# Optimization experiments

Hardware: AMD Instinct MI355X
Metric: run time of the kernel (lower is better)

The kernel has to match this reference:

```python
import jax, jax.numpy as jnp
import numpy as np

N0, N1 = 30000, 20000
N = N0 + N1
E = 400000
H0, H1, H2 = 4, 4, 1
DH = 64            # num_hidden
NC = 16            # num_classes
IN = 128           # per-type input feature dim
SLOPE = 0.2        # leaky relu negative slope


def setup_inputs() -> dict:
    key = jax.random.key(0)
    ks = iter(jax.random.split(key, 48))
    rn = lambda shape, s=0.05: jax.random.normal(next(ks), shape, jnp.float32) * s
    ri = lambda shape: jax.random.randint(next(ks), shape, 0, N, jnp.int32)
    inp = {
        'features0': rn((N0, IN), 1.0),
        'features1': rn((N1, IN), 1.0),
        'fc_w0': rn((IN, DH)), 'fc_b0': jnp.zeros((DH,), jnp.float32),
        'fc_w1': rn((IN, DH)), 'fc_b1': jnp.zeros((DH,), jnp.float32),
        'mix_w': jnp.zeros((2, 3, 2), jnp.float32),  # (n_types, num_layers+1, n_graphs)
        # GATConv params stacked over the 2 relation graphs
        'W0': rn((2, DH, H0 * DH)), 'al0': rn((2, H0, DH), 0.1), 'ar0': rn((2, H0, DH), 0.1), 'b0': jnp.zeros((2, H0 * DH), jnp.float32),
        'W1': rn((2, H0 * DH, H1 * DH)), 'al1': rn((2, H1, DH), 0.1), 'ar1': rn((2, H1, DH), 0.1), 'b1': jnp.zeros((2, H1 * DH), jnp.float32),
        'W2': rn((2, H1 * DH, H2 * NC)), 'al2': rn((2, H2, NC), 0.1), 'ar2': rn((2, H2, NC), 0.1), 'b2': jnp.zeros((2, H2 * NC), jnp.float32),
        'res2': rn((2, H1 * DH, H2 * NC)),  # res_fc for last layer (in != out*heads)
        'src0': ri((E,)), 'dst0': ri((E,)),
        'src1': ri((E,)), 'dst1': ri((E,)),
    }
    return inp


def gat_conv(h, src, dst, W, al, ar, b, H, D, res_mode, res_w, act):
    # h: (N, in)  ->  (N, H, D)
    feat = (h @ W).reshape(N, H, D)
    el = jnp.sum(feat * al, axis=-1)   # (N, H)
    er = jnp.sum(feat * ar, axis=-1)   # (N, H)
    e = jax.nn.leaky_relu(el[src] + er[dst], SLOPE)  # (E, H)
    # edge softmax over incoming edges of each dst node
    m = jax.ops.segment_max(e, dst, num_segments=N)
    ex = jnp.exp(e - m[dst])
    den = jax.ops.segment_sum(ex, dst, num_segments=N)
    alpha = ex / den[dst]                              # (E, H)
    out = jax.ops.segment_sum(feat[src] * alpha[..., None], dst, num_segments=N)
    if res_mode == 'id':
        out = out + h.reshape(N, H, D)
    elif res_mode == 'fc':
        out = out + (h @ res_w).reshape(N, H, D)
    out = out + b.reshape(1, H, D)
    return jax.nn.elu(out) if act else out


def _forward(features0, features1, fc_w0, fc_b0, fc_w1, fc_b1, mix_w,
             W0, al0, ar0, b0, W1, al1, ar1, b1, W2, al2, ar2, b2, res2,
             src0, dst0, src1, dst1):
    nt = jnp.concatenate([jnp.zeros(N0, jnp.int32), jnp.ones(N1, jnp.int32)])
    w = jax.nn.softmax(mix_w, axis=2)  # (types, layers+1, graphs)
    h = jnp.concatenate([features0 @ fc_w0 + fc_b0, features1 @ fc_w1 + fc_b1], axis=0)
    srcs, dsts = (src0, src1), (dst0, dst1)
    layers = [
        (W0, al0, ar0, b0, H0, DH, None, True),
        (W1, al1, ar1, b1, H1, DH, 'id', True),
    ]
    for l, (W, al, ar, b, H, D, rm, act) in enumerate(layers):
        acc = 0.
        for i in range(2):
            o = gat_conv(h, srcs[i], dsts[i], W[i], al[i], ar[i], b[i], H, D, rm, None, act)
            acc = acc + o.reshape(N, H * D) * w[nt, l, i][:, None]
        h = acc
    logits = 0.
    for i in range(2):
        o = gat_conv(h, srcs[i], dsts[i], W2[i], al2[i], ar2[i], b2[i], H2, NC, 'fc', res2[i], False)
        logits = logits + o.mean(axis=1) * w[nt, 2, i][:, None]
    return logits


def reference(features0, features1, fc_w0, fc_b0, fc_w1, fc_b1, mix_w,
              W0, al0, ar0, b0, W1, al1, ar1, b1, W2, al2, ar2, b2, res2,
              src0, dst0, src1, dst1):
    return _forward(features0, features1, fc_w0, fc_b0, fc_w1, fc_b1, mix_w,
                    W0, al0, ar0, b0, W1, al1, ar1, b1, W2, al2, ar2, b2, res2,
                    src0, dst0, src1, dst1)
```

## Files before the change

### kernel.cpp

```cpp
#include <hip/hip_runtime.h>
#include <hip/hip_bf16.h>

#define NN   50000
#define NN0  30000
#define EE   400000
#define NB_SCAN ((NN + 1023) / 1024)
#define NRT   3125
#define NGRP  ((NRT + 3) / 4)
#define NT0   1875

typedef unsigned short u16;
typedef unsigned int   u32;

typedef __attribute__((ext_vector_type(8))) __bf16 bf16x8;
typedef __attribute__((ext_vector_type(4))) float  f32x4;

__device__ __forceinline__ float bf2f(u16 u){ return __uint_as_float(((u32)u)<<16); }
__device__ __forceinline__ float lo16(u32 u){ return __uint_as_float(u<<16); }
__device__ __forceinline__ float hi16(u32 u){ return __uint_as_float(u & 0xffff0000u); }
__device__ __forceinline__ u16 f2bf(float f){
  u32 x = __float_as_uint(f);
  x += 0x7fffu + ((x>>16)&1u);
  return (u16)(x>>16);
}
__device__ __forceinline__ float elu_f(float x){ return x>0.f ? x : __expf(x)-1.f; }
__device__ __forceinline__ float lrelu(float x){ return x>0.f ? x : 0.2f*x; }
__device__ __forceinline__ bf16x8 ld_frag(const u16* p){
  uint4 v = *(const uint4*)p;
  return __builtin_bit_cast(bf16x8, v);
}
__device__ __forceinline__ bf16x8 cvt8(const float* p){
  float4 u = ((const float4*)p)[0];
  float4 v = ((const float4*)p)[1];
  u32 w0 = (u32)f2bf(u.x) | ((u32)f2bf(u.y)<<16);
  u32 w1 = (u32)f2bf(u.z) | ((u32)f2bf(u.w)<<16);
  u32 w2 = (u32)f2bf(v.x) | ((u32)f2bf(v.y)<<16);
  u32 w3 = (u32)f2bf(v.z) | ((u32)f2bf(v.w)<<16);
  uint4 r{w0,w1,w2,w3};
  return __builtin_bit_cast(bf16x8, r);
}

__global__ __launch_bounds__(256) void k_prep(
    const float* __restrict__ mix_w, float* __restrict__ wsoft,
    const float* __restrict__ W0, u16* __restrict__ W0p,
    const float* __restrict__ W1, u16* __restrict__ W1p,
    const float* __restrict__ W2, const float* __restrict__ res2, u16* __restrict__ W2p,
    const float* __restrict__ fcw0, const float* __restrict__ fcw1, u16* __restrict__ Fp,
    const float* __restrict__ al0, const float* __restrict__ ar0, u16* __restrict__ Vp)
{
  int t = blockIdx.x*256 + threadIdx.x;
  if (t < 6){
    float a0 = mix_w[t*2+0], a1 = mix_w[t*2+1];
    float mx = fmaxf(a0,a1);
    float e0 = __expf(a0-mx), e1 = __expf(a1-mx);
    wsoft[t*2+0] = e0/(e0+e1); wsoft[t*2+1] = e1/(e0+e1);
  }
  if (t < 4096){
    int gg = t>>11, fi = t&2047;
    int lane = fi&63, kb = (fi>>6)&1, ct = fi>>7;
    int q = lane>>4, c = lane&15;
    const float* src = W0 + (size_t)gg*16384;
    u16* o = W0p + (size_t)gg*16384 + (size_t)fi*8;
    #pragma unroll
    for (int j=0;j<8;j++) o[j] = f2bf(src[(size_t)(kb*32+q*8+j)*256 + ct*16 + c]);
  } else if (t < 20480){
    int u = t - 4096;
    int gg = u>>13, fi = u&8191;
    int lane = fi&63, kb = (fi>>6)&7, ct = fi>>9;
    int q = lane>>4, c = lane&15;
    const float* src = W1 + (size_t)gg*65536;
    u16* o = W1p + (size_t)gg*65536 + (size_t)fi*8;
    #pragma unroll
    for (int j=0;j<8;j++) o[j] = f2bf(src[(size_t)(kb*32+q*8+j)*256 + ct*16 + c]);
  } else if (t < 22528){
    int fi = t - 20480;
    int lane = fi&63, kb = (fi>>6)&7, ct = fi>>9;
    int q = lane>>4, c = lane&15;
    int cl = ct*16 + c;
    int i = cl>>5, which = (cl>>4)&1;
    const float* src = which ? res2 : W2;
    u16* o = W2p + (size_t)fi*8;
    #pragma unroll
    for (int j=0;j<8;j++) o[j] = f2bf(src[(size_t)i*4096 + (size_t)(kb*32+q*8+j)*16 + (cl&15)]);
  } else if (t < 24576){
    int u = t - 22528;
    int tt = u>>10, fi = u&1023;
    int lane = fi&63, kb = (fi>>6)&3, ct = fi>>8;
    int q = lane>>4, c = lane&15;
    const float* src = tt ? fcw1 : fcw0;
    u16* o = Fp + (size_t)tt*8192 + (size_t)fi*8;
    #pragma unroll
    for (int j=0;j<8;j++) o[j] = f2bf(src[(size_t)(kb*32+q*8+j)*64 + ct*16 + c]);
  } else if (t < 25600){
    int u = t - 24576;
    int fi = u>>3, j = u&7;
    int lane = fi&63, kb = fi>>6;
    int q = lane>>4, c = lane&15;
    int k = kb*32 + q*8 + j;
    int which = c>>3, g=(c>>2)&1, h=c&3;
    const float* sel = (which ? ar0 : al0) + (size_t)(g*4+h)*64;
    const float* Wrow = W0 + (size_t)g*16384 + (size_t)k*256 + h*64;
    float s=0.f;
    #pragma unroll 8
    for (int d=0;d<64;d++) s = fmaf(Wrow[d], sel[d], s);
    Vp[(size_t)fi*8 + j] = f2bf(s);
  }
}

__global__ void k_count2(const int* __restrict__ d0, const int* __restrict__ d1,
                         int* __restrict__ cnt2){
  int t = blockIdx.x*256 + threadIdx.x;
  int g = blockIdx.y;
  if (t < EE) atomicAdd(&cnt2[g*NN + (g ? d1[t] : d0[t])], 1);
}

__global__ __launch_bounds__(1024) void k_scan1(const int* __restrict__ cnt2,
                                                int* __restrict__ row2, int* __restrict__ bsum){
  __shared__ int wsum[16];
  int g = blockIdx.y;
  int lane = threadIdx.x & 63, wid = threadIdx.x >> 6;
  int i = blockIdx.x*1024 + threadIdx.x;
  int v = (i < NN) ? cnt2[g*NN + i] : 0;
  int x = v;
  #pragma unroll
  for (int off = 1; off < 64; off <<= 1){
    int y = __shfl_up(x, off, 64);
    if (lane >= off) x += y;
  }
  if (lane == 63) wsum[wid] = x;
  __syncthreads();
  if (wid == 0 && lane < 16){
    int s = wsum[lane];
    #pragma unroll
    for (int off = 1; off < 16; off <<= 1){
      int y = __shfl_up(s, off, 16);
      if (lane >= off) s += y;
    }
    wsum[lane] = s;
  }
  __syncthreads();
  int incl = x + (wid ? wsum[wid-1] : 0);
  if (i < NN) row2[(size_t)g*(NN+1) + i] = incl - v;
  if (threadIdx.x == 1023) bsum[g*NB_SCAN + blockIdx.x] = incl;
}

__global__ __launch_bounds__(128) void k_scan2(const int* __restrict__ bsum, int* __restrict__ boff){
  int g = threadIdx.x >> 6, lane = threadIdx.x & 63;
  int v = (lane < NB_SCAN) ? bsum[g*NB_SCAN + lane] : 0;
  int x = v;
  #pragma unroll
  for (int off = 1; off < 64; off <<= 1){
    int y = __shfl_up(x, off, 64);
    if (lane >= off) x += y;
  }
  if (lane < NB_SCAN) boff[g*NB_SCAN + lane] = x - v;
}

__global__ __launch_bounds__(1024) void k_scan3(int* __restrict__ row2, const int* __restrict__ boff){
  int g = blockIdx.y;
  int i = blockIdx.x*1024 + threadIdx.x;
  if (i < NN) row2[(size_t)g*(NN+1) + i] += boff[g*NB_SCAN + blockIdx.x];
  if (blockIdx.x == 0 && threadIdx.x == 0) row2[(size_t)g*(NN+1) + NN] = EE;
}

__global__ void k_scatter2(const int* __restrict__ s0, const int* __restrict__ d0,
                           const int* __restrict__ s1, const int* __restrict__ d1,
                           const int* __restrict__ row2, int* __restrict__ fill2,
                           u16* __restrict__ col2, u16* __restrict__ dstOf){
  int t = blockIdx.x*256 + threadIdx.x;
  int g = blockIdx.y;
  if (t >= EE) return;
  int d = g ? d1[t] : d0[t];
  int s = g ? s1[t] : s0[t];
  int pos = atomicAdd(&fill2[g*NN + d], 1);
  size_t slot = (size_t)g*EE + row2[(size_t)g*(NN+1) + d] + pos;
  col2[slot]  = (u16)s;
  dstOf[slot] = (u16)d;
}

__global__ void k_alpha4(const u16* __restrict__ col2, const u16* __restrict__ dstOf,
                         const float* __restrict__ el, const float* __restrict__ er,
                         size_t elStride, float* __restrict__ xbuf){
  int t = blockIdx.x*256 + threadIdx.x;
  int g = blockIdx.y;
  if (t >= EE) return;
  size_t slot = (size_t)g*EE + t;
  int s = col2[slot], d = dstOf[slot];
  const float* elg = el + (size_t)g*elStride;
  const float* erg = er + (size_t)g*elStride;
  float4 e4 = ((const float4*)elg)[s];
  float4 r4 = ((const float4*)erg)[d];
  float4 x;
  x.x = __expf(lrelu(e4.x + r4.x));
  x.y = __expf(lrelu(e4.y + r4.y));
  x.z = __expf(lrelu(e4.z + r4.z));
  x.w = __expf(lrelu(e4.w + r4.w));
  ((float4*)xbuf)[slot] = x;
}

__global__ void k_alpha1(const u16* __restrict__ col2, const u16* __restrict__ dstOf,
                         const float* __restrict__ el2, const float* __restrict__ er2,
                         float* __restrict__ xb2){
  int t = blockIdx.x*256 + threadIdx.x;
  int g = blockIdx.y;
  if (t >= EE) return;
  size_t slot = (size_t)g*EE + t;
  int s = col2[slot], d = dstOf[slot];
  xb2[slot] = __expf(lrelu(el2[(size_t)g*NN + s] + er2[(size_t)g*NN + d]));
}

__global__ __launch_bounds__(256) void k_inproj_m(
    const float* __restrict__ f0, const float* __restrict__ f1,
    const u16* __restrict__ Fp, const float* __restrict__ fb0, const float* __restrict__ fb1,
    u16* __restrict__ h0)
{
  int wv = threadIdx.x>>6, ln = threadIdx.x&63;
  int ti = blockIdx.x*4 + wv;
  if (ti >= NRT) return;
  int q = ln>>4, c = ln&15;
  int type = (ti < NT0) ? 0 : 1;
  const float* F = type ? f1 : f0;
  int rbase = type ? (ti*16 - NN0) : ti*16;
  const u16* Bg = Fp + (size_t)type*8192;
  const float* bb = type ? fb1 : fb0;
  f32x4 acc[4] = {};
  const float* Ap = F + (size_t)(rbase + c)*128;
  #pragma unroll
  for (int kb=0; kb<4; kb++){
    bf16x8 a = cvt8(Ap + kb*32 + q*8);
    #pragma unroll
    for (int ct=0; ct<4; ct++){
      bf16x8 b = ld_frag(Bg + ((size_t)(ct*4+kb)*64 + ln)*8);
      acc[ct] = __builtin_amdgcn_mfma_f32_16x16x32_bf16(a, b, acc[ct], 0,0,0);
    }
  }
  #pragma unroll
  for (int ct=0; ct<4; ct++){
    float bv = bb[ct*16+c];
    #pragma unroll
    for (int j=0;j<4;j++){
      int row = ti*16 + q*4 + j;
      h0[(size_t)row*64 + ct*16 + c] = f2bf(acc[ct][j] + bv);
    }
  }
}

__global__ __launch_bounds__(256) void k_eler0(
    const u16* __restrict__ h0, const u16* __restrict__ Vp,
    float* __restrict__ elA, float* __restrict__ erA)
{
  int wv = threadIdx.x>>6, ln = threadIdx.x&63;
  int ti = blockIdx.x*4 + wv;
  if (ti >= NRT) return;
  int q = ln>>4, c = ln&15;
  f32x4 acc = {};
  const u16* Ap = h0 + (size_t)(ti*16 + c)*64 + q*8;
  #pragma unroll
  for (int kb=0; kb<2; kb++){
    bf16x8 a = ld_frag(Ap + kb*32);
    bf16x8 b = ld_frag(Vp + ((size_t)(kb*64 + ln))*8);
    acc = __builtin_amdgcn_mfma_f32_16x16x32_bf16(a, b, acc, 0,0,0);
  }
  int which = c>>3, g = (c>>2)&1, h = c&3;
  float* dst = (which ? erA : elA) + (size_t)g*NN*4;
  #pragma unroll
  for (int j=0;j<4;j++){
    int row = ti*16 + q*4 + j;
    dst[row*4 + h] = acc[j];
  }
}

__global__ __launch_bounds__(256) void k_agg0(
    const int* __restrict__ row2, const u16* __restrict__ col2,
    const float* __restrict__ xbuf, const u16* __restrict__ h0,
    u16* __restrict__ aggB, size_t aggStride)
{
  int wv = threadIdx.x>>6, ln = threadIdx.x&63;
  int n = blockIdx.x*4 + wv;
  const int* rw0 = row2;
  const int* rw1 = row2 + (NN+1);
  const u16* cl0 = col2;
  const u16* cl1 = col2 + EE;
  const float4* xb0 = (const float4*)xbuf;
  const float4* xb1 = xb0 + EE;
  int b0_ = rw0[n], e0_ = rw0[n+1];
  int b1_ = rw1[n], e1_ = rw1[n+1];
  int k0 = b0_, k1 = b1_;
  float d00=0.f,d01=0.f,d02=0.f,d03=0.f, a00=0.f,a01=0.f,a02=0.f,a03=0.f;
  float d10=0.f,d11=0.f,d12=0.f,d13=0.f, a10=0.f,a11=0.f,a12=0.f,a13=0.f;
  while (k0+2<=e0_ && k1+2<=e1_){
    int sA=cl0[k0], sB=cl0[k0+1], sC=cl1[k1], sD=cl1[k1+1];
    float4 xA=xb0[k0], xB=xb0[k0+1], xC=xb1[k1], xD=xb1[k1+1];
    float vA=bf2f(h0[(size_t)sA*64+ln]);
    float vB=bf2f(h0[(size_t)sB*64+ln]);
    float vC=bf2f(h0[(size_t)sC*64+ln]);
    float vD=bf2f(h0[(size_t)sD*64+ln]);
    d00+=xA.x+xB.x; d01+=xA.y+xB.y; d02+=xA.z+xB.z; d03+=xA.w+xB.w;
    a00+=xA.x*vA+xB.x*vB; a01+=xA.y*vA+xB.y*vB;
    a02+=xA.z*vA+xB.z*vB; a03+=xA.w*vA+xB.w*vB;
    d10+=xC.x+xD.x; d11+=xC.y+xD.y; d12+=xC.z+xD.z; d13+=xC.w+xD.w;
    a10+=xC.x*vC+xD.x*vD; a11+=xC.y*vC+xD.y*vD;
    a12+=xC.z*vC+xD.z*vD; a13+=xC.w*vC+xD.w*vD;
    k0+=2; k1+=2;
  }
  for (; k0+2<=e0_; k0+=2){
    int sA=cl0[k0], sB=cl0[k0+1];
    float4 xA=xb0[k0], xB=xb0[k0+1];
    float vA=bf2f(h0[(size_t)sA*64+ln]);
    float vB=bf2f(h0[(size_t)sB*64+ln]);
    d00+=xA.x+xB.x; d01+=xA.y+xB.y; d02+=xA.z+xB.z; d03+=xA.w+xB.w;
    a00+=xA.x*vA+xB.x*vB; a01+=xA.y*vA+xB.y*vB;
    a02+=xA.z*vA+xB.z*vB; a03+=xA.w*vA+xB.w*vB;
  }
  for (; k0<e0_; k0++){
    int s=cl0[k0]; float4 x=xb0[k0];
    float v=bf2f(h0[(size_t)s*64+ln]);
    d00+=x.x; d01+=x.y; d02+=x.z; d03+=x.w;
    a00+=x.x*v; a01+=x.y*v; a02+=x.z*v; a03+=x.w*v;
  }
  for (; k1+2<=e1_; k1+=2){
    int sC=cl1[k1], sD=cl1[k1+1];
    float4 xC=xb1[k1], xD=xb1[k1+1];
    float vC=bf2f(h0[(size_t)sC*64+ln]);
    float vD=bf2f(h0[(size_t)sD*64+ln]);
    d10+=xC.x+xD.x; d11+=xC.y+xD.y; d12+=xC.z+xD.z; d13+=xC.w+xD.w;
    a10+=xC.x*vC+xD.x*vD; a11+=xC.y*vC+xD.y*vD;
    a12+=xC.z*vC+xD.z*vD; a13+=xC.w*vC+xD.w*vD;
  }
  for (; k1<e1_; k1++){
    int s=cl1[k1]; float4 x=xb1[k1];
    float v=bf2f(h0[(size_t)s*64+ln]);
    d10+=x.x; d11+=x.y; d12+=x.z; d13+=x.w;
    a10+=x.x*v; a11+=x.y*v; a12+=x.z*v; a13+=x.w*v;
  }
  bool hg0 = e0_ > b0_, hg1 = e1_ > b1_;
  u16* og0 = aggB + (size_t)n*256 + ln;
  og0[0]   = f2bf(hg0 ? a00/d00 : 0.f);
  og0[64]  = f2bf(hg0 ? a01/d01 : 0.f);
  og0[128] = f2bf(hg0 ? a02/d02 : 0.f);
  og0[192] = f2bf(hg0 ? a03/d03 : 0.f);
  u16* og1 = aggB + aggStride + (size_t)n*256 + ln;
  og1[0]   = f2bf(hg1 ? a10/d10 : 0.f);
  og1[64]  = f2bf(hg1 ? a11/d11 : 0.f);
  og1[128] = f2bf(hg1 ? a12/d12 : 0.f);
  og1[192] = f2bf(hg1 ? a13/d13 : 0.f);
}

__global__ __launch_bounds__(256) void k_head0(
    const u16* __restrict__ aggB, size_t aggStride,
    const u16* __restrict__ W0p, const float* __restrict__ b0,
    const float* __restrict__ wsoft, u16* __restrict__ h1)
{
  int wv = threadIdx.x>>6, ln = threadIdx.x&63;
  int ti = blockIdx.x*4 + wv;
  if (ti >= NRT) return;
  int q = ln>>4, c = ln&15;
  int type = (ti < NT0) ? 0 : 1;
  float wg0 = wsoft[type*6 + 0];
  float wg1 = wsoft[type*6 + 1];
  for (int h=0; h<4; h++){
    f32x4 acc[2][4] = {};
    #pragma unroll
    for (int g=0; g<2; g++){
      const u16* Ap = aggB + (size_t)g*aggStride + (size_t)(ti*16 + c)*256 + h*64 + q*8;
      const u16* Bg = W0p + (size_t)g*16384;
      #pragma unroll
      for (int kb=0; kb<2; kb++){
        bf16x8 a = ld_frag(Ap + kb*32);
        #pragma unroll
        for (int ct=0; ct<4; ct++){
          int ctg = h*4 + ct;
          bf16x8 b = ld_frag(Bg + ((size_t)(ctg*2 + kb)*64 + ln)*8);
          acc[g][ct] = __builtin_amdgcn_mfma_f32_16x16x32_bf16(a, b, acc[g][ct], 0,0,0);
        }
      }
    }
    #pragma unroll
    for (int ct=0; ct<4; ct++){
      int colg = h*64 + ct*16 + c;
      float bb0 = b0[colg], bb1 = b0[256 + colg];
      #pragma unroll
      for (int j=0;j<4;j++){
        int row = ti*16 + q*4 + j;
        float o = wg0*elu_f(acc[0][ct][j] + bb0) + wg1*elu_f(acc[1][ct][j] + bb1);
        h1[(size_t)row*256 + colg] = f2bf(o);
      }
    }
  }
}

template<int K>
__global__ __launch_bounds__(256) void k_gemm4(
    const u16* __restrict__ A,
    const u16* __restrict__ Bp, size_t bpStride,
    const float* __restrict__ al, const float* __restrict__ ar, int alStride,
    u16* __restrict__ feat, size_t featStride,
    float* __restrict__ el, float* __restrict__ er, size_t elStride)
{
  constexpr int KB = K/32;
  int wv = threadIdx.x>>6, ln = threadIdx.x&63;
  int bid = blockIdx.x;
  int g = bid / NGRP, grp = bid % NGRP;
  int split = wv, q = ln>>4, c = ln&15;
  const u16* Bpg = Bp + (size_t)g*bpStride;
  const float* alg = al + (size_t)g*alStride;
  const float* arg = ar + (size_t)g*alStride;
  u16* featg = feat + (size_t)g*featStride;
  float* elg = el + (size_t)g*elStride;
  float* erg = er + (size_t)g*elStride;

  f32x4 acc[4][4] = {};
  int  tbase = grp*4;
  bool valid[4];
  const u16* Ap[4];
  #pragma unroll
  for (int rt=0; rt<4; rt++){
    int ti = tbase + rt;
    valid[rt] = (ti < NRT);
    if (!valid[rt]) ti = NRT-1;
    Ap[rt] = A + (size_t)(ti*16 + c)*K + q*8;
  }
  const u16* Bbase = Bpg + ((size_t)(split*4)*KB*64 + ln)*8;

  #pragma unroll 2
  for (int kb=0; kb<KB; kb++){
    bf16x8 b[4], a[4];
    #pragma unroll
    for (int ct=0; ct<4; ct++) b[ct] = ld_frag(Bbase + (size_t)(ct*KB + kb)*64*8);
    #pragma unroll
    for (int rt=0; rt<4; rt++) a[rt] = ld_frag(Ap[rt] + kb*32);
    #pragma unroll
    for (int rt=0; rt<4; rt++)
      #pragma unroll
      for (int ct=0; ct<4; ct++)
        acc[rt][ct] = __builtin_amdgcn_mfma_f32_16x16x32_bf16(a[rt], b[ct], acc[rt][ct], 0,0,0);
  }

  float alv[4], arv[4];
  #pragma unroll
  for (int ct=0;ct<4;ct++){
    int cg = (split*4+ct)*16 + c;
    alv[ct] = alg[cg]; arv[ct] = arg[cg];
  }
  #pragma unroll
  for (int rt=0; rt<4; rt++){
    if (!valid[rt]) continue;
    int row0 = (tbase+rt)*16;
    #pragma unroll
    for (int j=0;j<4;j++){
      float ep=0.f, rp=0.f;
      #pragma unroll
      for (int ct=0;ct<4;ct++){ ep += acc[rt][ct][j]*alv[ct]; rp += acc[rt][ct][j]*arv[ct]; }
      #pragma unroll
      for (int off=8; off; off>>=1){ ep += __shfl_xor(ep,off,16); rp += __shfl_xor(rp,off,16); }
      int row = row0 + q*4 + j;
      if (c==0){ elg[row*4+split]=ep; erg[row*4+split]=rp; }
      #pragma unroll
      for (int ct=0;ct<4;ct++)
        featg[(size_t)row*256 + (split*4+ct)*16 + c] = f2bf(acc[rt][ct][j]);
    }
  }
}

template<int RES>
__global__ __launch_bounds__(256) void k_aggNF(
    const int* __restrict__ row2, const u16* __restrict__ col2,
    const float* __restrict__ xbuf,
    const u16* __restrict__ feat, size_t featStride,
    const u16* __restrict__ hres, const float* __restrict__ bias,
    const float* __restrict__ wsoft, int l,
    u16* __restrict__ hout)
{
  int wv = threadIdx.x>>6, ln = threadIdx.x&63;
  int n = blockIdx.x*4 + wv;
  int h = ln>>4;
  int type = (n<NN0)?0:1;
  float rx=0.f, ry=0.f, rz=0.f, rw_=0.f;
  if (RES){
    uint2 r = ((const uint2*)hres)[(size_t)n*64 + ln];
    rx=lo16(r.x); ry=hi16(r.x); rz=lo16(r.y); rw_=hi16(r.y);
  }
  const int* rw0 = row2;
  const int* rw1 = row2 + (NN+1);
  const u16* cl0 = col2;
  const u16* cl1 = col2 + EE;
  const float* x0p = xbuf;
  const float* x1p = xbuf + (size_t)EE*4;
  const uint2* fp0 = (const uint2*)feat;
  const uint2* fp1 = (const uint2*)(feat + featStride);
  int b0_ = rw0[n], e0_ = rw0[n+1];
  int b1_ = rw1[n], e1_ = rw1[n+1];
  int k0 = b0_, k1 = b1_;
  float den0=0.f, A0=0.f,A1=0.f,A2=0.f,A3=0.f;
  float den1=0.f, B0=0.f,B1=0.f,B2=0.f,B3=0.f;
  while (k0+4<=e0_ && k1+4<=e1_){
    int s0=cl0[k0], s1=cl0[k0+1], s2=cl0[k0+2], s3=cl0[k0+3];
    int t0=cl1[k1], t1=cl1[k1+1], t2=cl1[k1+2], t3=cl1[k1+3];
    float x0=x0p[(size_t)k0*4+h],     x1=x0p[(size_t)(k0+1)*4+h];
    float x2=x0p[(size_t)(k0+2)*4+h], x3=x0p[(size_t)(k0+3)*4+h];
    float y0=x1p[(size_t)k1*4+h],     y1=x1p[(size_t)(k1+1)*4+h];
    float y2=x1p[(size_t)(k1+2)*4+h], y3=x1p[(size_t)(k1+3)*4+h];
    uint2 f0=fp0[(size_t)s0*64+ln], f1=fp0[(size_t)s1*64+ln];
    uint2 f2=fp0[(size_t)s2*64+ln], f3=fp0[(size_t)s3*64+ln];
    uint2 g0=fp1[(size_t)t0*64+ln], g1=fp1[(size_t)t1*64+ln];
    uint2 g2=fp1[(size_t)t2*64+ln], g3=fp1[(size_t)t3*64+ln];
    den0 += (x0+x1) + (x2+x3);
    A0 += x0*lo16(f0.x)+x1*lo16(f1.x)+x2*lo16(f2.x)+x3*lo16(f3.x);
    A1 += x0*hi16(f0.x)+x1*hi16(f1.x)+x2*hi16(f2.x)+x3*hi16(f3.x);
    A2 += x0*lo16(f0.y)+x1*lo16(f1.y)+x2*lo16(f2.y)+x3*lo16(f3.y);
    A3 += x0*hi16(f0.y)+x1*hi16(f1.y)+x2*hi16(f2.y)+x3*hi16(f3.y);
    den1 += (y0+y1) + (y2+y3);
    B0 += y0*lo16(g0.x)+y1*lo16(g1.x)+y2*lo16(g2.x)+y3*lo16(g3.x);
    B1 += y0*hi16(g0.x)+y1*hi16(g1.x)+y2*hi16(g2.x)+y3*hi16(g3.x);
    B2 += y0*lo16(g0.y)+y1*lo16(g1.y)+y2*lo16(g2.y)+y3*lo16(g3.y);
    B3 += y0*hi16(g0.y)+y1*hi16(g1.y)+y2*hi16(g2.y)+y3*hi16(g3.y);
    k0+=4; k1+=4;
  }
  for (; k0+4<=e0_; k0+=4){
    int s0=cl0[k0], s1=cl0[k0+1], s2=cl0[k0+2], s3=cl0[k0+3];
    float x0=x0p[(size_t)k0*4+h],     x1=x0p[(size_t)(k0+1)*4+h];
    float x2=x0p[(size_t)(k0+2)*4+h], x3=x0p[(size_t)(k0+3)*4+h];
    uint2 f0=fp0[(size_t)s0*64+ln], f1=fp0[(size_t)s1*64+ln];
    uint2 f2=fp0[(size_t)s2*64+ln], f3=fp0[(size_t)s3*64+ln];
    den0 += (x0+x1) + (x2+x3);
    A0 += x0*lo16(f0.x)+x1*lo16(f1.x)+x2*lo16(f2.x)+x3*lo16(f3.x);
    A1 += x0*hi16(f0.x)+x1*hi16(f1.x)+x2*hi16(f2.x)+x3*hi16(f3.x);
    A2 += x0*lo16(f0.y)+x1*lo16(f1.y)+x2*lo16(f2.y)+x3*lo16(f3.y);
    A3 += x0*hi16(f0.y)+x1*hi16(f1.y)+x2*hi16(f2.y)+x3*hi16(f3.y);
  }
  for (; k0<e0_; k0++){
    int s=cl0[k0];
    float x=x0p[(size_t)k0*4+h];
    uint2 f=fp0[(size_t)s*64+ln];
    den0 += x;
    A0 += x*lo16(f.x); A1 += x*hi16(f.x); A2 += x*lo16(f.y); A3 += x*hi16(f.y);
  }
  for (; k1+4<=e1_; k1+=4){
    int t0=cl1[k1], t1=cl1[k1+1], t2=cl1[k1+2], t3=cl1[k1+3];
    float y0=x1p[(size_t)k1*4+h],     y1=x1p[(size_t)(k1+1)*4+h];
    float y2=x1p[(size_t)(k1+2)*4+h], y3=x1p[(size_t)(k1+3)*4+h];
    uint2 g0=fp1[(size_t)t0*64+ln], g1=fp1[(size_t)t1*64+ln];
    uint2 g2=fp1[(size_t)t2*64+ln], g3=fp1[(size_t)t3*64+ln];
    den1 += (y0+y1) + (y2+y3);
    B0 += y0*lo16(g0.x)+y1*lo16(g1.x)+y2*lo16(g2.x)+y3*lo16(g3.x);
    B1 += y0*hi16(g0.x)+y1*hi16(g1.x)+y2*hi16(g2.x)+y3*hi16(g3.x);
    B2 += y0*lo16(g0.y)+y1*lo16(g1.y)+y2*lo16(g2.y)+y3*lo16(g3.y);
    B3 += y0*hi16(g0.y)+y1*hi16(g1.y)+y2*hi16(g2.y)+y3*hi16(g3.y);
  }
  for (; k1<e1_; k1++){
    int t=cl1[k1];
    float y=x1p[(size_t)k1*4+h];
    uint2 g=fp1[(size_t)t*64+ln];
    den1 += y;
    B0 += y*lo16(g.x); B1 += y*hi16(g.x); B2 += y*lo16(g.y); B3 += y*hi16(g.y);
  }
  float inv0 = (e0_>b0_) ? 1.0f/den0 : 0.f;
  float inv1 = (e1_>b1_) ? 1.0f/den1 : 0.f;
  float4 bv0 = ((const float4*)(bias))[ln];
  float4 bv1 = ((const float4*)(bias + 256))[ln];
  float w0 = wsoft[type*6 + l*2 + 0];
  float w1 = wsoft[type*6 + l*2 + 1];
  float c0 = A0*inv0 + bv0.x, c1 = A1*inv0 + bv0.y, c2 = A2*inv0 + bv0.z, c3 = A3*inv0 + bv0.w;
  float e0 = B0*inv1 + bv1.x, e1 = B1*inv1 + bv1.y, e2 = B2*inv1 + bv1.z, e3 = B3*inv1 + bv1.w;
  if (RES){ c0+=rx; c1+=ry; c2+=rz; c3+=rw_; e0+=rx; e1+=ry; e2+=rz; e3+=rw_; }
  float o0 = w0*elu_f(c0) + w1*elu_f(e0);
  float o1 = w0*elu_f(c1) + w1*elu_f(e1);
  float o2 = w0*elu_f(c2) + w1*elu_f(e2);
  float o3 = w0*elu_f(c3) + w1*elu_f(e3);
  uint2 o;
  o.x = (u32)f2bf(o0) | ((u32)f2bf(o1)<<16);
  o.y = (u32)f2bf(o2) | ((u32)f2bf(o3)<<16);
  ((uint2*)hout)[(size_t)n*64 + ln] = o;
}

__global__ __launch_bounds__(256) void k_gemm2(
    const u16* __restrict__ A, const u16* __restrict__ Bp,
    const float* __restrict__ al2, const float* __restrict__ ar2,
    float* __restrict__ feat16, float* __restrict__ resb,
    float* __restrict__ el2, float* __restrict__ er2)
{
  int wv = threadIdx.x>>6, ln = threadIdx.x&63;
  int wt = blockIdx.x*4 + wv;
  if (wt >= NRT) return;
  int row0 = wt*16;
  int q = ln>>4, c = ln&15;
  f32x4 acc[4] = {};
  const u16* Ap = A + (size_t)(row0 + c)*256 + q*8;
  #pragma unroll
  for (int kb=0; kb<8; kb++){
    bf16x8 a = ld_frag(Ap + kb*32);
    #pragma unroll
    for (int t=0;t<4;t++){
      bf16x8 b = ld_frag(Bp + ((size_t)(t*8 + kb)*64 + ln)*8);
      acc[t] = __builtin_amdgcn_mfma_f32_16x16x32_bf16(a, b, acc[t], 0,0,0);
    }
  }
  #pragma unroll
  for (int i=0;i<2;i++){
    float alv = al2[i*16+c], arv = ar2[i*16+c];
    #pragma unroll
    for (int j=0;j<4;j++){
      float ep = acc[2*i][j]*alv, rp = acc[2*i][j]*arv;
      #pragma unroll
      for (int off=8; off; off>>=1){ ep += __shfl_xor(ep,off,16); rp += __shfl_xor(rp,off,16); }
      if (c==0){
        int row = row0 + q*4 + j;
        el2[(size_t)i*NN + row] = ep; er2[(size_t)i*NN + row] = rp;
      }
    }
    #pragma unroll
    for (int j=0;j<4;j++){
      int row = row0 + q*4 + j;
      feat16[(size_t)i*NN*16 + (size_t)row*16 + c] = acc[2*i][j];
      resb  [(size_t)i*NN*16 + (size_t)row*16 + c] = acc[2*i+1][j];
    }
  }
}

__global__ __launch_bounds__(256) void k_agg2D(
    const int* __restrict__ row2, const u16* __restrict__ col2,
    const float* __restrict__ xb2,
    const float* __restrict__ feat16, const float* __restrict__ resb,
    const float* __restrict__ b2, const float* __restrict__ wsoft,
    float* __restrict__ out)
{
  int t = threadIdx.x;
  int nl = t>>4, j = t&15;
  int n = blockIdx.x*16 + nl;
  int type = (n<NN0)?0:1;
  float o = 0.f;
  #pragma unroll
  for (int i=0;i<2;i++){
    const int* rw = row2 + (size_t)i*(NN+1);
    const u16* cl = col2 + (size_t)i*EE;
    const float* xb = xb2 + (size_t)i*EE;
    const float* f  = feat16 + (size_t)i*NN*16;
    int beg = rw[n], end = rw[n+1];
    float den = 0.f, acc = 0.f;
    int k = beg;
    for (; k+4<=end; k+=4){
      int s0=cl[k], s1=cl[k+1], s2=cl[k+2], s3=cl[k+3];
      float x0 = xb[k], x1 = xb[k+1], x2 = xb[k+2], x3 = xb[k+3];
      float v0 = f[(size_t)s0*16 + j];
      float v1 = f[(size_t)s1*16 + j];
      float v2 = f[(size_t)s2*16 + j];
      float v3 = f[(size_t)s3*16 + j];
      den += (x0+x1) + (x2+x3);
      acc += x0*v0 + x1*v1 + x2*v2 + x3*v3;
    }
    for (; k<end; k++){
      float x = xb[k];
      den += x;
      acc = fmaf(x, f[(size_t)cl[k]*16 + j], acc);
    }
    float inv = (end>beg) ? 1.0f/den : 0.f;
    float oi = acc*inv + b2[i*16+j] + resb[(size_t)i*NN*16 + (size_t)n*16 + j];
    o += oi * wsoft[type*6 + 4 + i];
  }
  out[(size_t)n*16 + j] = o;
}

extern "C" void kernel_launch(void* const* d_in, const int* in_sizes, int n_in,
                              void* d_out, int out_size, void* d_ws, size_t ws_size,
                              hipStream_t stream)
{
  const float* features0 = (const float*)d_in[0];
  const float* features1 = (const float*)d_in[1];
  const float* fc_w0 = (const float*)d_in[2];
  const float* fc_b0 = (const float*)d_in[3];
  const float* fc_w1 = (const float*)d_in[4];
  const float* fc_b1 = (const float*)d_in[5];
  const float* mix_w = (const float*)d_in[6];
  const float* W0  = (const float*)d_in[7];
  const float* al0 = (const float*)d_in[8];
  const float* ar0 = (const float*)d_in[9];
  const float* b0  = (const float*)d_in[10];
  const float* W1  = (const float*)d_in[11];
  const float* al1 = (const float*)d_in[12];
  const float* ar1 = (const float*)d_in[13];
  const float* b1  = (const float*)d_in[14];
  const float* W2  = (const float*)d_in[15];
  const float* al2 = (const float*)d_in[16];
  const float* ar2 = (const float*)d_in[17];
  const float* b2  = (const float*)d_in[18];
  const float* res2= (const float*)d_in[19];
  const int* src[2] = {(const int*)d_in[20], (const int*)d_in[22]};
  const int* dst[2] = {(const int*)d_in[21], (const int*)d_in[23]};
  (void)in_sizes; (void)n_in; (void)out_size; (void)ws_size;

  char* ws = (char*)d_ws;
  size_t off = 0;
  auto alloc = [&](size_t bytes)->char*{
    char* p = ws + off; off += (bytes + 255) & ~(size_t)255; return p;
  };
  float* wsoft = (float*)alloc(64*4);
  u16*   W0p   = (u16*)  alloc((size_t)2*64*256*2);
  u16*   W1p   = (u16*)  alloc((size_t)2*256*256*2);
  u16*   W2p   = (u16*)  alloc((size_t)256*64*2);
  u16*   Fp    = (u16*)  alloc((size_t)2*128*64*2);
  u16*   Vp    = (u16*)  alloc((size_t)64*16*2);
  int*   row2  = (int*)  alloc((size_t)2*(NN+1)*4);
  u16*   col2  = (u16*)  alloc((size_t)2*EE*2);
  u16*   dstOf = (u16*)  alloc((size_t)2*EE*2);
  int*   zeros = (int*)  alloc((size_t)4*NN*4);
  int*   cnt2  = zeros;
  int*   fill2 = zeros + 2*NN;
  int*   bsum  = (int*)alloc((size_t)2*NB_SCAN*4);
  int*   boff  = (int*)alloc((size_t)2*NB_SCAN*4);
  u16*   h0    = (u16*)alloc((size_t)NN*64*2);
  u16*   h1    = (u16*)alloc((size_t)NN*256*2);
  u16*   h2    = (u16*)alloc((size_t)NN*256*2);
  float* elA   = (float*)alloc((size_t)2*NN*4*4);
  float* erA   = (float*)alloc((size_t)2*NN*4*4);
  float* xbuf  = (float*)alloc((size_t)2*EE*4*4);
  size_t featStride = (size_t)NN*256;
  size_t off_D = off;
  u16* regionD = (u16*)alloc(2*featStride*2);
  u16* aggB  = regionD;
  u16* featD = regionD;
  float* feat16 = (float*)(ws + off_D);
  float* resb   = feat16 + (size_t)2*NN*16;
  float* el2    = resb   + (size_t)2*NN*16;
  float* er2    = el2    + (size_t)2*NN;

  k_prep<<<100,256,0,stream>>>(mix_w, wsoft, W0, W0p, W1, W1p, W2, res2, W2p,
                               fc_w0, fc_w1, Fp, al0, ar0, Vp);

  hipMemsetAsync(zeros, 0, (size_t)4*NN*4, stream);
  {
    dim3 gEb((EE+255)/256, 2), gS(NB_SCAN, 2);
    k_count2 <<<gEb,256,0,stream>>>(dst[0], dst[1], cnt2);
    k_scan1  <<<gS,1024,0,stream>>>(cnt2, row2, bsum);
    k_scan2  <<<1,128,0,stream>>>(bsum, boff);
    k_scan3  <<<gS,1024,0,stream>>>(row2, boff);
    k_scatter2<<<gEb,256,0,stream>>>(src[0], dst[0], src[1], dst[1], row2, fill2, col2, dstOf);
  }

  k_inproj_m<<<NGRP,256,0,stream>>>(features0, features1, Fp, fc_b0, fc_b1, h0);
  k_eler0   <<<NGRP,256,0,stream>>>(h0, Vp, elA, erA);

  dim3 gE((EE+255)/256, 2);

  k_alpha4<<<gE,256,0,stream>>>(col2, dstOf, elA, erA, (size_t)NN*4, xbuf);
  k_agg0 <<<NN/4,256,0,stream>>>(row2, col2, xbuf, h0, aggB, featStride);
  k_head0<<<NGRP,256,0,stream>>>(aggB, featStride, W0p, b0, wsoft, h1);

  k_gemm4<256><<<2*NGRP,256,0,stream>>>(h1, W1p, (size_t)256*256, al1, ar1, 256,
                                        featD, featStride, elA, erA, (size_t)NN*4);
  k_alpha4<<<gE,256,0,stream>>>(col2, dstOf, elA, erA, (size_t)NN*4, xbuf);
  k_aggNF<1><<<NN/4,256,0,stream>>>(row2, col2, xbuf, featD, featStride,
                                    h1, b1, wsoft, 1, h2);

  k_gemm2<<<NGRP,256,0,stream>>>(h2, W2p, al2, ar2, feat16, resb, el2, er2);
  k_alpha1<<<gE,256,0,stream>>>(col2, dstOf, el2, er2, xbuf);
  k_agg2D<<<NN/16,256,0,stream>>>(row2, col2, xbuf, feat16, resb, b2, wsoft, (float*)d_out);
}
```

Measured before the change: 458.8 us.

## Fuse launches: fold el/er projection into input GEMM, inline last-layer alpha

```diff
diff --git a/kernel.cpp b/kernel.cpp
--- a/kernel.cpp
+++ b/kernel.cpp
@@ -46,9 +46,10 @@
     const float* __restrict__ W1, u16* __restrict__ W1p,
     const float* __restrict__ W2, const float* __restrict__ res2, u16* __restrict__ W2p,
     const float* __restrict__ fcw0, const float* __restrict__ fcw1, u16* __restrict__ Fp,
-    const float* __restrict__ al0, const float* __restrict__ ar0, u16* __restrict__ Vp)
+    int* __restrict__ zeros)
 {
   int t = blockIdx.x*256 + threadIdx.x;
+  for (int z = t; z < 4*NN; z += gridDim.x*256) zeros[z] = 0;
   if (t < 6){
     float a0 = mix_w[t*2+0], a1 = mix_w[t*2+1];
     float mx = fmaxf(a0,a1);
@@ -91,19 +92,42 @@
     u16* o = Fp + (size_t)tt*8192 + (size_t)fi*8;
     #pragma unroll
     for (int j=0;j<8;j++) o[j] = f2bf(src[(size_t)(kb*32+q*8+j)*64 + ct*16 + c]);
-  } else if (t < 25600){
-    int u = t - 24576;
-    int fi = u>>3, j = u&7;
-    int lane = fi&63, kb = fi>>6;
-    int q = lane>>4, c = lane&15;
-    int k = kb*32 + q*8 + j;
-    int which = c>>3, g=(c>>2)&1, h=c&3;
-    const float* sel = (which ? ar0 : al0) + (size_t)(g*4+h)*64;
-    const float* Wrow = W0 + (size_t)g*16384 + (size_t)k*256 + h*64;
-    float s=0.f;
+  }
+}
+
+__global__ __launch_bounds__(128) void k_prep2(
+    const float* __restrict__ W0,
+    const float* __restrict__ al0, const float* __restrict__ ar0,
+    const float* __restrict__ fcw0, const float* __restrict__ fcw1,
+    const float* __restrict__ fcb0, const float* __restrict__ fcb1,
+    u16* __restrict__ V2p, float* __restrict__ bV)
+{
+  __shared__ float V[64];
+  int b = blockIdx.x;
+  int tt = b>>4, cl = b&15;
+  int which = cl>>3, g = (cl>>2)&1, h = cl&3;
+  int t = threadIdx.x;
+  const float* sel = (which ? ar0 : al0) + (size_t)(g*4+h)*64;
+  if (t < 64){
+    const float* Wrow = W0 + (size_t)g*16384 + (size_t)t*256 + h*64;
+    float s = 0.f;
     #pragma unroll 8
-    for (int d=0;d<64;d++) s = fmaf(Wrow[d], sel[d], s);
-    Vp[(size_t)fi*8 + j] = f2bf(s);
+    for (int d=0; d<64; d++) s = fmaf(Wrow[d], sel[d], s);
+    V[t] = s;
+  }
+  __syncthreads();
+  const float* fw = tt ? fcw1 : fcw0;
+  float s = 0.f;
+  #pragma unroll 8
+  for (int d=0; d<64; d++) s = fmaf(fw[(size_t)t*64 + d], V[d], s);
+  int kb = t>>5, q = (t>>3)&3, j = t&7;
+  V2p[(size_t)tt*2048 + ((size_t)kb*64 + q*16 + cl)*8 + j] = f2bf(s);
+  if (t == 0){
+    const float* fbp = tt ? fcb1 : fcb0;
+    float sb = 0.f;
+    #pragma unroll 8
+    for (int d=0; d<64; d++) sb = fmaf(fbp[d], V[d], sb);
+    bV[tt*16 + cl] = sb;
   }
 }
 
@@ -144,22 +168,20 @@
   if (threadIdx.x == 1023) bsum[g*NB_SCAN + blockIdx.x] = incl;
 }
 
-__global__ __launch_bounds__(128) void k_scan2(const int* __restrict__ bsum, int* __restrict__ boff){
-  int g = threadIdx.x >> 6, lane = threadIdx.x & 63;
-  int v = (lane < NB_SCAN) ? bsum[g*NB_SCAN + lane] : 0;
-  int x = v;
-  #pragma unroll
-  for (int off = 1; off < 64; off <<= 1){
-    int y = __shfl_up(x, off, 64);
-    if (lane >= off) x += y;
-  }
-  if (lane < NB_SCAN) boff[g*NB_SCAN + lane] = x - v;
-}
-
-__global__ __launch_bounds__(1024) void k_scan3(int* __restrict__ row2, const int* __restrict__ boff){
+__global__ __launch_bounds__(1024) void k_scan3(int* __restrict__ row2,
+                                                const int* __restrict__ bsum){
+  __shared__ int base;
   int g = blockIdx.y;
+  if (threadIdx.x < 64){
+    int lane = threadIdx.x;
+    int v = (lane < (int)blockIdx.x) ? bsum[g*NB_SCAN + lane] : 0;
+    #pragma unroll
+    for (int off = 32; off; off >>= 1) v += __shfl_xor(v, off, 64);
+    if (lane == 0) base = v;
+  }
+  __syncthreads();
   int i = blockIdx.x*1024 + threadIdx.x;
-  if (i < NN) row2[(size_t)g*(NN+1) + i] += boff[g*NB_SCAN + blockIdx.x];
+  if (i < NN) row2[(size_t)g*(NN+1) + i] += base;
   if (blockIdx.x == 0 && threadIdx.x == 0) row2[(size_t)g*(NN+1) + NN] = EE;
 }
 
@@ -198,21 +220,11 @@
   ((float4*)xbuf)[slot] = x;
 }
 
-__global__ void k_alpha1(const u16* __restrict__ col2, const u16* __restrict__ dstOf,
-                         const float* __restrict__ el2, const float* __restrict__ er2,
-                         float* __restrict__ xb2){
-  int t = blockIdx.x*256 + threadIdx.x;
-  int g = blockIdx.y;
-  if (t >= EE) return;
-  size_t slot = (size_t)g*EE + t;
-  int s = col2[slot], d = dstOf[slot];
-  xb2[slot] = __expf(lrelu(el2[(size_t)g*NN + s] + er2[(size_t)g*NN + d]));
-}
-
 __global__ __launch_bounds__(256) void k_inproj_m(
     const float* __restrict__ f0, const float* __restrict__ f1,
     const u16* __restrict__ Fp, const float* __restrict__ fb0, const float* __restrict__ fb1,
-    u16* __restrict__ h0)
+    const u16* __restrict__ V2p, const float* __restrict__ bV,
+    u16* __restrict__ h0, float* __restrict__ elA, float* __restrict__ erA)
 {
   int wv = threadIdx.x>>6, ln = threadIdx.x&63;
   int ti = blockIdx.x*4 + wv;
@@ -222,8 +234,10 @@
   const float* F = type ? f1 : f0;
   int rbase = type ? (ti*16 - NN0) : ti*16;
   const u16* Bg = Fp + (size_t)type*8192;
+  const u16* Vg = V2p + (size_t)type*2048;
   const float* bb = type ? fb1 : fb0;
   f32x4 acc[4] = {};
+  f32x4 accE = {};
   const float* Ap = F + (size_t)(rbase + c)*128;
   #pragma unroll
   for (int kb=0; kb<4; kb++){
@@ -233,40 +247,25 @@
       bf16x8 b = ld_frag(Bg + ((size_t)(ct*4+kb)*64 + ln)*8);
       acc[ct] = __builtin_amdgcn_mfma_f32_16x16x32_bf16(a, b, acc[ct], 0,0,0);
     }
+    bf16x8 bv_ = ld_frag(Vg + ((size_t)kb*64 + ln)*8);
+    accE = __builtin_amdgcn_mfma_f32_16x16x32_bf16(a, bv_, accE, 0,0,0);
   }
   #pragma unroll
   for (int ct=0; ct<4; ct++){
-    float bv = bb[ct*16+c];
+    float bvs = bb[ct*16+c];
     #pragma unroll
     for (int j=0;j<4;j++){
       int row = ti*16 + q*4 + j;
-      h0[(size_t)row*64 + ct*16 + c] = f2bf(acc[ct][j] + bv);
-    }
-  }
-}
-
-__global__ __launch_bounds__(256) void k_eler0(
-    const u16* __restrict__ h0, const u16* __restrict__ Vp,
-    float* __restrict__ elA, float* __restrict__ erA)
-{
-  int wv = threadIdx.x>>6, ln = threadIdx.x&63;
-  int ti = blockIdx.x*4 + wv;
-  if (ti >= NRT) return;
-  int q = ln>>4, c = ln&15;
-  f32x4 acc = {};
-  const u16* Ap = h0 + (size_t)(ti*16 + c)*64 + q*8;
-  #pragma unroll
-  for (int kb=0; kb<2; kb++){
-    bf16x8 a = ld_frag(Ap + kb*32);
-    bf16x8 b = ld_frag(Vp + ((size_t)(kb*64 + ln))*8);
-    acc = __builtin_amdgcn_mfma_f32_16x16x32_bf16(a, b, acc, 0,0,0);
-  }
-  int which = c>>3, g = (c>>2)&1, h = c&3;
-  float* dst = (which ? erA : elA) + (size_t)g*NN*4;
+      h0[(size_t)row*64 + ct*16 + c] = f2bf(acc[ct][j] + bvs);
+    }
+  }
+  int which = c>>3, gg = (c>>2)&1, hh = c&3;
+  float bVv = bV[type*16 + c];
+  float* dst = (which ? erA : elA) + (size_t)gg*NN*4;
   #pragma unroll
   for (int j=0;j<4;j++){
     int row = ti*16 + q*4 + j;
-    dst[row*4 + h] = acc[j];
+    dst[row*4 + hh] = accE[j] + bVv;
   }
 }
 
@@ -619,7 +618,7 @@
 
 __global__ __launch_bounds__(256) void k_agg2D(
     const int* __restrict__ row2, const u16* __restrict__ col2,
-    const float* __restrict__ xb2,
+    const float* __restrict__ el2, const float* __restrict__ er2,
     const float* __restrict__ feat16, const float* __restrict__ resb,
     const float* __restrict__ b2, const float* __restrict__ wsoft,
     float* __restrict__ out)
@@ -633,14 +632,18 @@
   for (int i=0;i<2;i++){
     const int* rw = row2 + (size_t)i*(NN+1);
     const u16* cl = col2 + (size_t)i*EE;
-    const float* xb = xb2 + (size_t)i*EE;
+    const float* elg = el2 + (size_t)i*NN;
+    float ern = er2[(size_t)i*NN + n];
     const float* f  = feat16 + (size_t)i*NN*16;
     int beg = rw[n], end = rw[n+1];
     float den = 0.f, acc = 0.f;
     int k = beg;
     for (; k+4<=end; k+=4){
       int s0=cl[k], s1=cl[k+1], s2=cl[k+2], s3=cl[k+3];
-      float x0 = xb[k], x1 = xb[k+1], x2 = xb[k+2], x3 = xb[k+3];
+      float x0 = __expf(lrelu(elg[s0] + ern));
+      float x1 = __expf(lrelu(elg[s1] + ern));
+      float x2 = __expf(lrelu(elg[s2] + ern));
+      float x3 = __expf(lrelu(elg[s3] + ern));
       float v0 = f[(size_t)s0*16 + j];
       float v1 = f[(size_t)s1*16 + j];
       float v2 = f[(size_t)s2*16 + j];
@@ -649,9 +652,10 @@
       acc += x0*v0 + x1*v1 + x2*v2 + x3*v3;
     }
     for (; k<end; k++){
-      float x = xb[k];
+      int s = cl[k];
+      float x = __expf(lrelu(elg[s] + ern));
       den += x;
-      acc = fmaf(x, f[(size_t)cl[k]*16 + j], acc);
+      acc = fmaf(x, f[(size_t)s*16 + j], acc);
     }
     float inv = (end>beg) ? 1.0f/den : 0.f;
     float oi = acc*inv + b2[i*16+j] + resb[(size_t)i*NN*16 + (size_t)n*16 + j];
@@ -698,7 +702,8 @@
   u16*   W1p   = (u16*)  alloc((size_t)2*256*256*2);
   u16*   W2p   = (u16*)  alloc((size_t)256*64*2);
   u16*   Fp    = (u16*)  alloc((size_t)2*128*64*2);
-  u16*   Vp    = (u16*)  alloc((size_t)64*16*2);
+  u16*   V2p   = (u16*)  alloc((size_t)2*128*16*2);
+  float* bV    = (float*)alloc((size_t)32*4);
   int*   row2  = (int*)  alloc((size_t)2*(NN+1)*4);
   u16*   col2  = (u16*)  alloc((size_t)2*EE*2);
   u16*   dstOf = (u16*)  alloc((size_t)2*EE*2);
@@ -706,7 +711,6 @@
   int*   cnt2  = zeros;
   int*   fill2 = zeros + 2*NN;
   int*   bsum  = (int*)alloc((size_t)2*NB_SCAN*4);
-  int*   boff  = (int*)alloc((size_t)2*NB_SCAN*4);
   u16*   h0    = (u16*)alloc((size_t)NN*64*2);
   u16*   h1    = (u16*)alloc((size_t)NN*256*2);
   u16*   h2    = (u16*)alloc((size_t)NN*256*2);
@@ -724,20 +728,19 @@
   float* er2    = el2    + (size_t)2*NN;
 
   k_prep<<<100,256,0,stream>>>(mix_w, wsoft, W0, W0p, W1, W1p, W2, res2, W2p,
-                               fc_w0, fc_w1, Fp, al0, ar0, Vp);
-
-  hipMemsetAsync(zeros, 0, (size_t)4*NN*4, stream);
+                               fc_w0, fc_w1, Fp, zeros);
+  k_prep2<<<32,128,0,stream>>>(W0, al0, ar0, fc_w0, fc_w1, fc_b0, fc_b1, V2p, bV);
+
   {
     dim3 gEb((EE+255)/256, 2), gS(NB_SCAN, 2);
     k_count2 <<<gEb,256,0,stream>>>(dst[0], dst[1], cnt2);
     k_scan1  <<<gS,1024,0,stream>>>(cnt2, row2, bsum);
-    k_scan2  <<<1,128,0,stream>>>(bsum, boff);
-    k_scan3  <<<gS,1024,0,stream>>>(row2, boff);
+    k_scan3  <<<gS,1024,0,stream>>>(row2, bsum);
     k_scatter2<<<gEb,256,0,stream>>>(src[0], dst[0], src[1], dst[1], row2, fill2, col2, dstOf);
   }
 
-  k_inproj_m<<<NGRP,256,0,stream>>>(features0, features1, Fp, fc_b0, fc_b1, h0);
-  k_eler0   <<<NGRP,256,0,stream>>>(h0, Vp, elA, erA);
+  k_inproj_m<<<NGRP,256,0,stream>>>(features0, features1, Fp, fc_b0, fc_b1,
+                                    V2p, bV, h0, elA, erA);
 
   dim3 gE((EE+255)/256, 2);
 
@@ -752,6 +755,5 @@
                                     h1, b1, wsoft, 1, h2);
 
   k_gemm2<<<NGRP,256,0,stream>>>(h2, W2p, al2, ar2, feat16, resb, el2, er2);
-  k_alpha1<<<gE,256,0,stream>>>(col2, dstOf, el2, er2, xbuf);
-  k_agg2D<<<NN/16,256,0,stream>>>(row2, col2, xbuf, feat16, resb, b2, wsoft, (float*)d_out);
-}
+  k_agg2D<<<NN/16,256,0,stream>>>(row2, col2, el2, er2, feat16, resb, b2, wsoft, (float*)d_out);
+}
```

Result: no change. 455.4 us (-0.7%).
